# Kernel tuning notes

Hardware: AMD Instinct MI355X
Metric: run time of the kernel (lower is better)

Reference implementation:

```python
import jax, jax.numpy as jnp
import numpy as np

B, S = 16, 32768
LEVELS = (5, 20)
TIME_DIM = 8
NUM_FREQS = 6  # frequency xyz encoder: 3*(1+2*6)=39 dims
HID = 128
IN_DIM = 3 * (1 + 2 * NUM_FREQS) + 2 * TIME_DIM  # 55


def setup_inputs() -> dict:
    key = jax.random.key(0)
    ks = jax.random.split(key, 16)
    time = jax.random.uniform(ks[0], (B,), dtype=jnp.float32)
    xyz = jax.random.uniform(ks[1], (B, S, 3), dtype=jnp.float32) * 2.0 - 1.0  # in [-1,1]
    te0 = jax.random.normal(ks[2], (LEVELS[0] + 1, TIME_DIM), dtype=jnp.float32)
    te1 = jax.random.normal(ks[3], (LEVELS[1] + 1, TIME_DIM), dtype=jnp.float32)
    W0 = jax.random.normal(ks[4], (IN_DIM, HID), dtype=jnp.float32) * 0.05
    b0 = jnp.zeros((HID,), dtype=jnp.float32)
    W1 = jax.random.normal(ks[5], (HID, HID), dtype=jnp.float32) * 0.05
    b1 = jnp.zeros((HID,), dtype=jnp.float32)
    W2 = jax.random.normal(ks[6], (HID, HID), dtype=jnp.float32) * 0.05
    b2 = jnp.zeros((HID,), dtype=jnp.float32)
    Wout = jax.random.normal(ks[7], (HID, 1), dtype=jnp.float32) * 0.05
    bout = jnp.zeros((1,), dtype=jnp.float32)
    return {"time": time, "xyz": xyz, "te0": te0, "te1": te1,
            "W0": W0, "b0": b0, "W1": W1, "b1": b1, "W2": W2, "b2": b2,
            "Wout": Wout, "bout": bout}


def _time_encode(t, emb, L):
    # bucketize t into L uniform intervals on [0,1), lerp between bucket endpoints
    tL = t * L
    idx = jnp.clip(jnp.floor(tL).astype(jnp.int32), 0, L - 1)  # (B,)
    w = (idx + 1).astype(t.dtype) - tL                          # weight for lower endpoint
    lerped = w[:, None] * emb[idx] + (1.0 - w)[:, None] * emb[idx + 1]
    # t >= 1: use last embedding directly (torch fallback branch)
    return jnp.where((t >= 1.0)[:, None], emb[L][None, :], lerped)


def _xyz_encode(x):
    # frequency encoding, include_input, freqs 2^0..2^(NUM_FREQS-1)
    freqs = jnp.asarray(2.0 ** np.arange(NUM_FREQS), dtype=x.dtype)  # (F,)
    xp = x[:, None, :] * freqs[None, :, None]                         # (N, F, 3)
    n = x.shape[0]
    return jnp.concatenate([x, jnp.sin(xp).reshape(n, -1), jnp.cos(xp).reshape(n, -1)], axis=-1)


def reference(time, xyz, te0, te1, W0, b0, W1, b1, W2, b2, Wout, bout):
    s = xyz.shape[1]
    t_enc = jnp.concatenate([_time_encode(time, te0, LEVELS[0]),
                             _time_encode(time, te1, LEVELS[1])], axis=-1)  # (B, 16)
    t_enc = jnp.repeat(t_enc, s, axis=0)          # (B*S, 16)  'B d -> (B S) d'
    pts = (xyz.reshape(-1, 3) + 1.0) / 2.0        # (B*S, 3)
    x = jnp.concatenate([t_enc, _xyz_encode(pts)], axis=1)  # (B*S, 55)
    x = jax.nn.relu(x @ W0 + b0)
    x = jax.nn.relu(x @ W1 + b1)
    x = jax.nn.relu(x @ W2 + b2)
    return x @ Wout + bout  # (B*S, 1)
```

## Files before the change

kernel.cpp:

```cpp
#include <hip/hip_runtime.h>

typedef _Float16 f16;
typedef __attribute__((ext_vector_type(2))) __fp16 fp16x2;
typedef __attribute__((ext_vector_type(8))) _Float16 f16x8;
typedef __attribute__((ext_vector_type(4))) float f32x4;
typedef __attribute__((ext_vector_type(4))) unsigned int u32x4;

#define NPTS   (16 * 32768)
#define W0P_OFF 0
#define W1P_OFF (16 * 1024)
#define W2P_OFF (48 * 1024)
#define WOP_OFF (80 * 1024)
#define FRAGS_BYTES (84 * 1024)
#define TENC_OFF FRAGS_BYTES
#define WS_NEEDED (FRAGS_BYTES + 1024)
#define LDS_TOTAL 4096

__global__ void pack_weights(const float* __restrict__ time, const float* __restrict__ te0,
                             const float* __restrict__ te1, const float* __restrict__ W0,
                             const float* __restrict__ W1, const float* __restrict__ W2,
                             const float* __restrict__ Wout, unsigned char* __restrict__ ws) {
  const int bi = blockIdx.x;
  const int l = threadIdx.x;
  const int g = l >> 4, r16 = l & 15;
  if (bi < 84) {
    const float* W; int obase, fi, kt, mt, kmax; bool natural, outcol;
    if (bi < 16)      { W = W0;   fi = bi;      mt = fi >> 1; kt = fi & 1; obase = W0P_OFF; kmax = 55;  natural = true;  outcol = false; }
    else if (bi < 48) { W = W1;   fi = bi - 16; mt = fi >> 2; kt = fi & 3; obase = W1P_OFF; kmax = 128; natural = false; outcol = false; }
    else if (bi < 80) { W = W2;   fi = bi - 48; mt = fi >> 2; kt = fi & 3; obase = W2P_OFF; kmax = 128; natural = false; outcol = false; }
    else              { W = Wout; fi = bi - 80; mt = 0;       kt = fi;     obase = WOP_OFF; kmax = 128; natural = false; outcol = true;  }
    const int m = mt * 16 + r16;
    f16 vals[8] __attribute__((aligned(16)));
#pragma unroll
    for (int j = 0; j < 8; ++j) {
      const int k = natural ? (kt * 32 + g * 8 + j)
                            : (kt * 32 + (j >> 2) * 16 + g * 4 + (j & 3));
      float v = 0.f;
      if (k < kmax) v = outcol ? ((m == 0) ? Wout[k] : 0.f) : W[k * 128 + m];
      vals[j] = (f16)v;
    }
    *(u32x4*)(ws + obase + (fi * 64 + l) * 16) = *(const u32x4*)vals;
  } else {
    const int idx = (bi - 84) * 64 + l;
    const int b = idx >> 4, d = idx & 15;
    const float t = time[b];
    const float* emb; int L, dd;
    if (d < 8) { emb = te0; L = 5;  dd = d; }
    else       { emb = te1; L = 20; dd = d - 8; }
    const float tL = t * (float)L;
    int i = (int)floorf(tL);
    i = i < 0 ? 0 : (i > L - 1 ? L - 1 : i);
    const float wlo = (float)(i + 1) - tL;
    float v = wlo * emb[i * 8 + dd] + (1.f - wlo) * emb[(i + 1) * 8 + dd];
    if (t >= 1.f) v = emb[L * 8 + dd];
    ((float*)(ws + TENC_OFF))[idx] = v;
  }
}

__device__ __forceinline__ unsigned int pkmax0(unsigned int x) {
  unsigned int r;
  asm("v_pk_max_f16 %0, %1, %2" : "=v"(r) : "v"(x), "v"(0u));
  return r;
}
__device__ __forceinline__ unsigned int pkrtz(float a, float b) {
  union { fp16x2 h; unsigned int u; } c;
  c.h = __builtin_amdgcn_cvt_pkrtz(a, b);
  return c.u;
}

template <int KT>
__device__ __forceinline__ void layer_swapped(const unsigned char* __restrict__ wsrc,
                                              const float* __restrict__ bias,
                                              const f16x8 (&Bin)[KT][4], f16x8 (&Bout)[4][4],
                                              int lane) {
  const int g4 = (lane >> 4) * 4;
  f16x8 A0b[3], A1b[3];
  float4 ba, bb;
  f32x4 acc[2][4];
#pragma unroll
  for (int s = 0; s < 2; ++s) {
    const int mtp = s / KT, kt = s % KT;
    A0b[s] = *(const f16x8*)(wsrc + (((2 * mtp)     * KT + kt) * 64 + lane) * 16);
    A1b[s] = *(const f16x8*)(wsrc + (((2 * mtp + 1) * KT + kt) * 64 + lane) * 16);
  }
#pragma unroll
  for (int s = 0; s < 4 * KT; ++s) {
    const int mtp = s / KT, kt = s % KT, cb = s % 3;
    if (kt == 0) {
      ba = *(const float4*)(bias + mtp * 32 + g4);
      bb = *(const float4*)(bias + mtp * 32 + 16 + g4);
#pragma unroll
      for (int nt = 0; nt < 4; ++nt) {
        acc[0][nt] = (f32x4){ba.x, ba.y, ba.z, ba.w};
        acc[1][nt] = (f32x4){bb.x, bb.y, bb.z, bb.w};
      }
    }
    if (s + 2 < 4 * KT) {
      const int mtp2 = (s + 2) / KT, kt2 = (s + 2) % KT, pb = (s + 2) % 3;
      A0b[pb] = *(const f16x8*)(wsrc + (((2 * mtp2)     * KT + kt2) * 64 + lane) * 16);
      A1b[pb] = *(const f16x8*)(wsrc + (((2 * mtp2 + 1) * KT + kt2) * 64 + lane) * 16);
    }
    __builtin_amdgcn_s_setprio(1);
#pragma unroll
    for (int nt = 0; nt < 4; ++nt)
      acc[0][nt] = __builtin_amdgcn_mfma_f32_16x16x32_f16(A0b[cb], Bin[kt][nt], acc[0][nt], 0, 0, 0);
#pragma unroll
    for (int nt = 0; nt < 4; ++nt)
      acc[1][nt] = __builtin_amdgcn_mfma_f32_16x16x32_f16(A1b[cb], Bin[kt][nt], acc[1][nt], 0, 0, 0);
    __builtin_amdgcn_s_setprio(0);
    if (kt == KT - 1) {
#pragma unroll
      for (int nt = 0; nt < 4; ++nt) {
        union { unsigned int w[4]; f16x8 v; } u;
        u.w[0] = pkmax0(pkrtz(acc[0][nt][0], acc[0][nt][1]));
        u.w[1] = pkmax0(pkrtz(acc[0][nt][2], acc[0][nt][3]));
        u.w[2] = pkmax0(pkrtz(acc[1][nt][0], acc[1][nt][1]));
        u.w[3] = pkmax0(pkrtz(acc[1][nt][2], acc[1][nt][3]));
        Bout[mtp][nt] = u.v;
      }
    }
  }
}

__global__ void __launch_bounds__(64, 1)
mlp_main(const float* __restrict__ xyz, const float* __restrict__ b0,
         const float* __restrict__ b1, const float* __restrict__ b2,
         const float* __restrict__ bout, const unsigned char* __restrict__ ws,
         float* __restrict__ out) {
  extern __shared__ char lds[];
  const int lane = threadIdx.x;
  const int g = lane >> 4, r16 = lane & 15;

  char* scr = lds;
  const float bo = bout[0];

  const int pbase = blockIdx.x * 64;
  const int p = pbase + lane;

  float ff[64];
  const float* tb = (const float*)(ws + TENC_OFF) + (blockIdx.x >> 9) * 16;
#pragma unroll
  for (int i = 0; i < 16; ++i) ff[i] = tb[i];
  const float xs0 = xyz[p * 3], xs1 = xyz[p * 3 + 1], xs2 = xyz[p * 3 + 2];
  const float pcs[3] = {(xs0 + 1.f) * 0.5f, (xs1 + 1.f) * 0.5f, (xs2 + 1.f) * 0.5f};
#pragma unroll
  for (int c = 0; c < 3; ++c) {
    ff[16 + c] = pcs[c];
    float s = __sinf(pcs[c]), co = __cosf(pcs[c]);
#pragma unroll
    for (int f = 0; f < 6; ++f) {
      ff[19 + f * 3 + c] = s;
      ff[37 + f * 3 + c] = co;
      const float s2 = 2.f * s * co, c2 = 1.f - 2.f * s * s;
      s = s2; co = c2;
    }
  }
#pragma unroll
  for (int i = 55; i < 64; ++i) ff[i] = 0.f;
  unsigned int fw[32];
#pragma unroll
  for (int i = 0; i < 32; ++i) fw[i] = pkrtz(ff[2 * i], ff[2 * i + 1]);

  f16x8 B0[2][4];
#pragma unroll
  for (int h = 0; h < 2; ++h) {
    if ((lane >> 5) == h) {
#pragma unroll
      for (int s = 0; s < 8; ++s)
        *(u32x4*)(scr + (lane & 31) * 128 + ((s ^ (lane & 7)) * 16)) = ((const u32x4*)fw)[s];
    }
    asm volatile("s_waitcnt lgkmcnt(0)" ::: "memory");
#pragma unroll
    for (int kt = 0; kt < 2; ++kt)
#pragma unroll
      for (int nn = 0; nn < 2; ++nn) {
        const int row = nn * 16 + r16;
        B0[kt][h * 2 + nn] = *(const f16x8*)(scr + row * 128 + (((4 * kt + g) ^ (row & 7)) * 16));
      }
    asm volatile("s_waitcnt lgkmcnt(0)" ::: "memory");
  }

  f16x8 Bx[4][4], By[4][4];
  layer_swapped<2>(ws + W0P_OFF, b0, B0, Bx, lane);
  layer_swapped<4>(ws + W1P_OFF, b1, Bx, By, lane);
  layer_swapped<4>(ws + W2P_OFF, b2, By, Bx, lane);

  f16x8 Ab[4];
#pragma unroll
  for (int kt = 0; kt < 4; ++kt)
    Ab[kt] = *(const f16x8*)(ws + WOP_OFF + (kt * 64 + lane) * 16);
  const f32x4 bovec = (f32x4){bo, bo, bo, bo};
  f32x4 accO[4];
  __builtin_amdgcn_s_setprio(1);
#pragma unroll
  for (int nt = 0; nt < 4; ++nt)
    accO[nt] = __builtin_amdgcn_mfma_f32_16x16x32_f16(Ab[0], Bx[0][nt], bovec, 0, 0, 0);
#pragma unroll
  for (int kt = 1; kt < 4; ++kt) {
#pragma unroll
    for (int nt = 0; nt < 4; ++nt)
      accO[nt] = __builtin_amdgcn_mfma_f32_16x16x32_f16(Ab[kt], Bx[kt][nt], accO[nt], 0, 0, 0);
  }
  __builtin_amdgcn_s_setprio(0);

  const float a0 = __shfl(accO[0][0], r16, 64);
  const float a1 = __shfl(accO[1][0], r16, 64);
  const float a2 = __shfl(accO[2][0], r16, 64);
  const float a3 = __shfl(accO[3][0], r16, 64);
  const float v = g == 0 ? a0 : g == 1 ? a1 : g == 2 ? a2 : a3;
  out[pbase + lane] = v;
}

extern "C" void kernel_launch(void* const* d_in, const int* in_sizes, int n_in,
                              void* d_out, int out_size, void* d_ws, size_t ws_size,
                              hipStream_t stream) {
  const float* time = (const float*)d_in[0];
  const float* xyz  = (const float*)d_in[1];
  const float* te0  = (const float*)d_in[2];
  const float* te1  = (const float*)d_in[3];
  const float* W0   = (const float*)d_in[4];
  const float* b0   = (const float*)d_in[5];
  const float* W1   = (const float*)d_in[6];
  const float* b1   = (const float*)d_in[7];
  const float* W2   = (const float*)d_in[8];
  const float* b2   = (const float*)d_in[9];
  const float* Wout = (const float*)d_in[10];
  const float* bout = (const float*)d_in[11];
  float* out = (float*)d_out;
  unsigned char* ws = (unsigned char*)d_ws;
  if (ws_size < WS_NEEDED) return;

  pack_weights<<<88, 64, 0, stream>>>(time, te0, te1, W0, W1, W2, Wout, ws);
  mlp_main<<<NPTS / 64, 64, LDS_TOTAL, stream>>>(xyz, b0, b1, b2, bout, ws, out);
}
```

Measured before the change: 46.75 us.

## Fold time encoding into per-batch layer-0 bias and use hardware sin/cos

The 16 time-encoding features are constant within a batch, so their contribution through W0 is precomputed in the pack kernel as a per-batch effective bias (b0 + t_enc·W0). The main kernel then feeds only the 39 xyz features into layer 0, which removes loads of the time encoding and shrinks the live feature array. It also replaces __sinf/__cosf with direct v_sin/v_cos instructions on pre-scaled revolutions. The K dimension of layer 0 stays padded to 64, so the MFMA count does not change, and the precomputed bias is kept in fp32, which slightly changes rounding compared with quantising the time features to fp16.

```diff
diff --git a/kernel.cpp b/kernel.cpp
--- a/kernel.cpp
+++ b/kernel.cpp
@@ -12,20 +12,21 @@
 #define W2P_OFF (48 * 1024)
 #define WOP_OFF (80 * 1024)
 #define FRAGS_BYTES (84 * 1024)
-#define TENC_OFF FRAGS_BYTES
-#define WS_NEEDED (FRAGS_BYTES + 1024)
+#define B0E_OFF FRAGS_BYTES
+#define WS_NEEDED (FRAGS_BYTES + 8192)
 #define LDS_TOTAL 4096
 
 __global__ void pack_weights(const float* __restrict__ time, const float* __restrict__ te0,
                              const float* __restrict__ te1, const float* __restrict__ W0,
-                             const float* __restrict__ W1, const float* __restrict__ W2,
-                             const float* __restrict__ Wout, unsigned char* __restrict__ ws) {
+                             const float* __restrict__ b0, const float* __restrict__ W1,
+                             const float* __restrict__ W2, const float* __restrict__ Wout,
+                             unsigned char* __restrict__ ws) {
   const int bi = blockIdx.x;
   const int l = threadIdx.x;
   const int g = l >> 4, r16 = l & 15;
   if (bi < 84) {
     const float* W; int obase, fi, kt, mt, kmax; bool natural, outcol;
-    if (bi < 16)      { W = W0;   fi = bi;      mt = fi >> 1; kt = fi & 1; obase = W0P_OFF; kmax = 55;  natural = true;  outcol = false; }
+    if (bi < 16)      { W = W0;   fi = bi;      mt = fi >> 1; kt = fi & 1; obase = W0P_OFF; kmax = 39;  natural = true;  outcol = false; }
     else if (bi < 48) { W = W1;   fi = bi - 16; mt = fi >> 2; kt = fi & 3; obase = W1P_OFF; kmax = 128; natural = false; outcol = false; }
     else if (bi < 80) { W = W2;   fi = bi - 48; mt = fi >> 2; kt = fi & 3; obase = W2P_OFF; kmax = 128; natural = false; outcol = false; }
     else              { W = Wout; fi = bi - 80; mt = 0;       kt = fi;     obase = WOP_OFF; kmax = 128; natural = false; outcol = true;  }
@@ -36,24 +37,33 @@
       const int k = natural ? (kt * 32 + g * 8 + j)
                             : (kt * 32 + (j >> 2) * 16 + g * 4 + (j & 3));
       float v = 0.f;
-      if (k < kmax) v = outcol ? ((m == 0) ? Wout[k] : 0.f) : W[k * 128 + m];
+      if (k < kmax) {
+        if (outcol)       v = (m == 0) ? Wout[k] : 0.f;
+        else if (natural) v = W[(16 + k) * 128 + m];
+        else              v = W[k * 128 + m];
+      }
       vals[j] = (f16)v;
     }
     *(u32x4*)(ws + obase + (fi * 64 + l) * 16) = *(const u32x4*)vals;
   } else {
     const int idx = (bi - 84) * 64 + l;
-    const int b = idx >> 4, d = idx & 15;
+    const int b = idx >> 7, m = idx & 127;
     const float t = time[b];
-    const float* emb; int L, dd;
-    if (d < 8) { emb = te0; L = 5;  dd = d; }
-    else       { emb = te1; L = 20; dd = d - 8; }
-    const float tL = t * (float)L;
-    int i = (int)floorf(tL);
-    i = i < 0 ? 0 : (i > L - 1 ? L - 1 : i);
-    const float wlo = (float)(i + 1) - tL;
-    float v = wlo * emb[i * 8 + dd] + (1.f - wlo) * emb[(i + 1) * 8 + dd];
-    if (t >= 1.f) v = emb[L * 8 + dd];
-    ((float*)(ws + TENC_OFF))[idx] = v;
+    float acc = b0[m];
+#pragma unroll
+    for (int d = 0; d < 16; ++d) {
+      const float* emb; int L, dd;
+      if (d < 8) { emb = te0; L = 5;  dd = d; }
+      else       { emb = te1; L = 20; dd = d - 8; }
+      const float tL = t * (float)L;
+      int i = (int)floorf(tL);
+      i = i < 0 ? 0 : (i > L - 1 ? L - 1 : i);
+      const float wlo = (float)(i + 1) - tL;
+      float v = wlo * emb[i * 8 + dd] + (1.f - wlo) * emb[(i + 1) * 8 + dd];
+      if (t >= 1.f) v = emb[L * 8 + dd];
+      acc += v * W0[d * 128 + m];
+    }
+    ((float*)(ws + B0E_OFF))[b * 128 + m] = acc;
   }
 }
 
@@ -66,6 +76,12 @@
   union { fp16x2 h; unsigned int u; } c;
   c.h = __builtin_amdgcn_cvt_pkrtz(a, b);
   return c.u;
+}
+__device__ __forceinline__ float hwsin_rev(float rev) {
+  float r; asm("v_sin_f32 %0, %1" : "=v"(r) : "v"(rev)); return r;
+}
+__device__ __forceinline__ float hwcos_rev(float rev) {
+  float r; asm("v_cos_f32 %0, %1" : "=v"(r) : "v"(rev)); return r;
 }
 
 template <int KT>
@@ -123,10 +139,9 @@
 }
 
 __global__ void __launch_bounds__(64, 1)
-mlp_main(const float* __restrict__ xyz, const float* __restrict__ b0,
-         const float* __restrict__ b1, const float* __restrict__ b2,
-         const float* __restrict__ bout, const unsigned char* __restrict__ ws,
-         float* __restrict__ out) {
+mlp_main(const float* __restrict__ xyz, const float* __restrict__ b1,
+         const float* __restrict__ b2, const float* __restrict__ bout,
+         const unsigned char* __restrict__ ws, float* __restrict__ out) {
   extern __shared__ char lds[];
   const int lane = threadIdx.x;
   const int g = lane >> 4, r16 = lane & 15;
@@ -137,29 +152,29 @@
   const int pbase = blockIdx.x * 64;
   const int p = pbase + lane;
 
-  float ff[64];
-  const float* tb = (const float*)(ws + TENC_OFF) + (blockIdx.x >> 9) * 16;
-#pragma unroll
-  for (int i = 0; i < 16; ++i) ff[i] = tb[i];
+  float ff[40];
   const float xs0 = xyz[p * 3], xs1 = xyz[p * 3 + 1], xs2 = xyz[p * 3 + 2];
   const float pcs[3] = {(xs0 + 1.f) * 0.5f, (xs1 + 1.f) * 0.5f, (xs2 + 1.f) * 0.5f};
+  const float INV2PI = 0.15915494309189535f;
 #pragma unroll
   for (int c = 0; c < 3; ++c) {
-    ff[16 + c] = pcs[c];
-    float s = __sinf(pcs[c]), co = __cosf(pcs[c]);
+    ff[c] = pcs[c];
+    const float rev = pcs[c] * INV2PI;
+    float s = hwsin_rev(rev), co = hwcos_rev(rev);
 #pragma unroll
     for (int f = 0; f < 6; ++f) {
-      ff[19 + f * 3 + c] = s;
-      ff[37 + f * 3 + c] = co;
+      ff[3 + f * 3 + c] = s;
+      ff[21 + f * 3 + c] = co;
       const float s2 = 2.f * s * co, c2 = 1.f - 2.f * s * s;
       s = s2; co = c2;
     }
   }
-#pragma unroll
-  for (int i = 55; i < 64; ++i) ff[i] = 0.f;
+  ff[39] = 0.f;
   unsigned int fw[32];
 #pragma unroll
-  for (int i = 0; i < 32; ++i) fw[i] = pkrtz(ff[2 * i], ff[2 * i + 1]);
+  for (int i = 0; i < 20; ++i) fw[i] = pkrtz(ff[2 * i], ff[2 * i + 1]);
+#pragma unroll
+  for (int i = 20; i < 32; ++i) fw[i] = 0u;
 
   f16x8 B0[2][4];
 #pragma unroll
@@ -180,8 +195,9 @@
     asm volatile("s_waitcnt lgkmcnt(0)" ::: "memory");
   }
 
+  const float* b0e = (const float*)(ws + B0E_OFF) + (blockIdx.x >> 9) * 128;
   f16x8 Bx[4][4], By[4][4];
-  layer_swapped<2>(ws + W0P_OFF, b0, B0, Bx, lane);
+  layer_swapped<2>(ws + W0P_OFF, b0e, B0, Bx, lane);
   layer_swapped<4>(ws + W1P_OFF, b1, Bx, By, lane);
   layer_swapped<4>(ws + W2P_OFF, b2, By, Bx, lane);
 
@@ -230,6 +246,6 @@
   unsigned char* ws = (unsigned char*)d_ws;
   if (ws_size < WS_NEEDED) return;
 
-  pack_weights<<<88, 64, 0, stream>>>(time, te0, te1, W0, W1, W2, Wout, ws);
-  mlp_main<<<NPTS / 64, 64, LDS_TOTAL, stream>>>(xyz, b0, b1, b2, bout, ws, out);
-}
+  pack_weights<<<116, 64, 0, stream>>>(time, te0, te1, W0, b0, W1, W2, Wout, ws);
+  mlp_main<<<NPTS / 64, 64, LDS_TOTAL, stream>>>(xyz, b1, b2, bout, ws, out);
+}
```

New measurement: 46.87 us. Within noise of the previous version (+0.3%).
